# Kernel tuning notes

Hardware: AMD Instinct MI355X
Metric: run time of the kernel (lower is better)

The kernel has to match this reference:

```python
import jax, jax.numpy as jnp
import numpy as np

B, S, N = 8, 64, 256
STATE, IN_F, OUT_F = 128, 64, 64
ALPHA = 0.2
NEG = -9e15


def setup_inputs() -> dict:
    key = jax.random.key(0)
    ks = jax.random.split(key, 12)
    d = {
        "hyper_inputs": jax.random.normal(ks[0], (B, S, STATE), jnp.float32),
        "inputs": jax.random.normal(ks[1], (B, S, N, IN_F), jnp.float32),
        "Adj": jax.random.randint(ks[2], (N, N), 0, 2, jnp.int32),
        # hyper_w: Linear(STATE,32) -> ReLU -> Linear(32, OUT_F*IN_F)
        "w1": jax.random.normal(ks[3], (STATE, 32), jnp.float32) * 0.08,
        "b1": jax.random.normal(ks[4], (32,), jnp.float32) * 0.01,
        "w2": jax.random.normal(ks[5], (32, OUT_F * IN_F), jnp.float32) * 0.08,
        "b2": jax.random.normal(ks[6], (OUT_F * IN_F,), jnp.float32) * 0.01,
        # hyper_a: Linear(STATE,32) -> ReLU -> Linear(32, 2*OUT_F)
        "aw1": jax.random.normal(ks[7], (STATE, 32), jnp.float32) * 0.08,
        "ab1": jax.random.normal(ks[8], (32,), jnp.float32) * 0.01,
        "aw2": jax.random.normal(ks[9], (32, 2 * OUT_F), jnp.float32) * 0.08,
        "ab2": jax.random.normal(ks[10], (2 * OUT_F,), jnp.float32) * 0.01,
    }
    return d


def _leaky(x):
    return jnp.where(x >= 0, x, ALPHA * x)


def reference(hyper_inputs, inputs, Adj, w1, b1, w2, b2, aw1, ab1, aw2, ab2):
    # hypernetwork-generated per-(b,s) weights
    hdn = jax.nn.relu(hyper_inputs @ w1 + b1)            # [B,S,32]
    W = jnp.abs(hdn @ w2 + b2).reshape(B, S, IN_F, OUT_F)
    hda = jax.nn.relu(hyper_inputs @ aw1 + ab1)
    a = jnp.abs(hda @ aw2 + ab2)                          # [B,S,2*OUT_F]

    h = jnp.einsum('bsni,bsio->bsno', inputs, W)          # [B,S,N,OUT_F]

    # decomposed GAT scores: e[b,s,i,j] = leakyrelu(h_i.a1 + h_j.a2)
    a1, a2 = a[..., :OUT_F], a[..., OUT_F:]
    e1 = jnp.einsum('bsno,bso->bsn', h, a1)               # source term
    e2 = jnp.einsum('bsno,bso->bsn', h, a2)               # target term
    e = _leaky(e1[..., :, None] + e2[..., None, :])       # [B,S,N,N]

    attention = jnp.where(Adj > 0, e, NEG)
    # NOTE: faithful to original: softmax over dim=1 (the S axis)
    attention = jax.nn.softmax(attention, axis=1)
    h_prime = jnp.einsum('bsij,bsjo->bsio', attention, h)  # [B,S,N,OUT_F]
    return jax.nn.elu(h_prime)                              # concat=True branch
```

## Files before the change

kernel.cpp:

```cpp
#include <hip/hip_runtime.h>
#include <hip/hip_bf16.h>
#include <math.h>

#define BB 8
#define SS 64
#define NN 256
#define ST 128
#define IF 64
#define OF 64
#define H1 32
#define ALPHA 0.2f
#define LOG2E 1.4426950408889634f

typedef short short8 __attribute__((ext_vector_type(8)));
typedef short short4_t __attribute__((ext_vector_type(4)));
typedef float f32x4 __attribute__((ext_vector_type(4)));
typedef unsigned short ushort_t;

static __device__ __forceinline__ ushort_t f2bf(float f) {
    __hip_bfloat16 h = __float2bfloat16(f);
    return *reinterpret_cast<ushort_t*>(&h);
}

__global__ __launch_bounds__(512) void k_hyper2(
    const float* __restrict__ hyper,
    const float* __restrict__ w1, const float* __restrict__ b1,
    const float* __restrict__ w2, const float* __restrict__ b2,
    const float* __restrict__ aw1, const float* __restrict__ ab1,
    const float* __restrict__ aw2, const float* __restrict__ ab2,
    float* __restrict__ Wd, float* __restrict__ Aa)
{
    const int t = threadIdx.x;
    const int bs0 = blockIdx.x * 2;
    __shared__ float hy[2][ST];
    __shared__ float hdn_s[2][H1];
    __shared__ float hda_s[2][H1];
    if (t < 2 * ST)
        hy[t >> 7][t & 127] = hyper[(size_t)bs0 * ST + t];
    __syncthreads();
    if (t < 64) {
        const int q = t >> 5, c = t & 31;
        float acc = b1[c];
#pragma unroll 4
        for (int k = 0; k < ST; ++k) acc = fmaf(hy[q][k], w1[k * H1 + c], acc);
        hdn_s[q][c] = fmaxf(acc, 0.f);
    } else if (t < 128) {
        const int tt = t - 64;
        const int q = tt >> 5, c = tt & 31;
        float acc = ab1[c];
#pragma unroll 4
        for (int k = 0; k < ST; ++k) acc = fmaf(hy[q][k], aw1[k * H1 + c], acc);
        hda_s[q][c] = fmaxf(acc, 0.f);
    }
    __syncthreads();
    if (t < 256) {
        const int q = t >> 7, c = t & 127;
        float a = ab2[c];
#pragma unroll
        for (int k = 0; k < H1; ++k)
            a = fmaf(hda_s[q][k], aw2[k * 128 + c], a);
        Aa[(size_t)(bs0 + q) * 128 + c] = fabsf(a);
    }
#pragma unroll
    for (int p = 0; p < 2; ++p) {
        const int e = t * 4 + p * 2048;
        const float4 bb = *(const float4*)&b2[e];
        float4 a0 = bb, a1 = bb;
#pragma unroll
        for (int kq = 0; kq < 8; ++kq) {
            const float4 h0 = *(const float4*)&hdn_s[0][kq * 4];
            const float4 h1 = *(const float4*)&hdn_s[1][kq * 4];
#pragma unroll
            for (int c = 0; c < 4; ++c) {
                const float4 wv = *(const float4*)&w2[(size_t)(kq * 4 + c) * 4096 + e];
                const float s0 = (c == 0) ? h0.x : (c == 1) ? h0.y : (c == 2) ? h0.z : h0.w;
                const float s1 = (c == 0) ? h1.x : (c == 1) ? h1.y : (c == 2) ? h1.z : h1.w;
                a0.x = fmaf(s0, wv.x, a0.x); a0.y = fmaf(s0, wv.y, a0.y);
                a0.z = fmaf(s0, wv.z, a0.z); a0.w = fmaf(s0, wv.w, a0.w);
                a1.x = fmaf(s1, wv.x, a1.x); a1.y = fmaf(s1, wv.y, a1.y);
                a1.z = fmaf(s1, wv.z, a1.z); a1.w = fmaf(s1, wv.w, a1.w);
            }
        }
        a0.x = fabsf(a0.x); a0.y = fabsf(a0.y); a0.z = fabsf(a0.z); a0.w = fabsf(a0.w);
        a1.x = fabsf(a1.x); a1.y = fabsf(a1.y); a1.z = fabsf(a1.z); a1.w = fabsf(a1.w);
        *(float4*)&Wd[(size_t)(bs0 + 0) * 4096 + e] = a0;
        *(float4*)&Wd[(size_t)(bs0 + 1) * 4096 + e] = a1;
    }
}

__global__ __launch_bounds__(256) void k_h(
    const float* __restrict__ x, const float* __restrict__ Wd,
    const float* __restrict__ Aa,
    ushort_t* __restrict__ HbT, float* __restrict__ E1, float* __restrict__ E2)
{
    const int bs = blockIdx.x;
    const int tid = threadIdx.x;
    const int wid = tid >> 6;
    const int lane = tid & 63;
    const int l15 = lane & 15;
    const int lhi = lane >> 4;

    __shared__ ushort_t Wt[IF * OF];
    __shared__ float wa1s[IF], wa2s[IF];
    __shared__ float a1s[OF], a2s[OF];

    if (tid < 64) a1s[tid] = Aa[(size_t)bs * 128 + tid];
    else if (tid < 128) a2s[tid - 64] = Aa[(size_t)bs * 128 + tid];

    {
        const float4* w4 = (const float4*)(Wd + (size_t)bs * 4096);
#pragma unroll
        for (int p = 0; p < 4; ++p) {
            const int idx = tid + p * 256;
            const float4 f = w4[idx];
            const int k = (idx * 4) >> 6;
            const int o0 = (idx * 4) & 63;
            Wt[(o0 + 0) * 64 + (k ^ (((o0 + 0) & 7) << 3))] = f2bf(f.x);
            Wt[(o0 + 1) * 64 + (k ^ (((o0 + 1) & 7) << 3))] = f2bf(f.y);
            Wt[(o0 + 2) * 64 + (k ^ (((o0 + 2) & 7) << 3))] = f2bf(f.z);
            Wt[(o0 + 3) * 64 + (k ^ (((o0 + 3) & 7) << 3))] = f2bf(f.w);
        }
    }
    __syncthreads();

    if (tid < 64) {
        const float4* wr = (const float4*)(Wd + (size_t)bs * 4096 + tid * 64);
        float s1 = 0.f, s2 = 0.f;
#pragma unroll
        for (int q = 0; q < 16; ++q) {
            const float4 f = wr[q];
            const float4 u = *(const float4*)&a1s[q * 4];
            const float4 v = *(const float4*)&a2s[q * 4];
            s1 += f.x * u.x + f.y * u.y + f.z * u.z + f.w * u.w;
            s2 += f.x * v.x + f.y * v.y + f.z * v.z + f.w * v.w;
        }
        wa1s[tid] = s1; wa2s[tid] = s2;
    }
    __syncthreads();

    {
        const float4* xr = (const float4*)(x + ((size_t)bs * NN + tid) * IF);
        float s1 = 0.f, s2 = 0.f;
#pragma unroll
        for (int q = 0; q < 16; ++q) {
            const float4 f = xr[q];
            const float4 u = *(const float4*)&wa1s[q * 4];
            const float4 v = *(const float4*)&wa2s[q * 4];
            s1 += f.x * u.x + f.y * u.y + f.z * u.z + f.w * u.w;
            s2 += f.x * v.x + f.y * v.y + f.z * v.z + f.w * v.w;
        }
        E1[(size_t)bs * NN + tid] = s1 * LOG2E;
        E2[(size_t)bs * NN + tid] = s2 * LOG2E;
    }

    f32x4 acc[4][4];
#pragma unroll
    for (int mt = 0; mt < 4; ++mt)
#pragma unroll
        for (int nt = 0; nt < 4; ++nt) acc[mt][nt] = (f32x4){0.f, 0.f, 0.f, 0.f};

    short8 af[4][2];
#pragma unroll
    for (int mt = 0; mt < 4; ++mt) {
        const int row = wid * 64 + mt * 16 + l15;
        const float* xrow = x + ((size_t)bs * NN + row) * IF;
#pragma unroll
        for (int ks = 0; ks < 2; ++ks) {
            const int k0 = ks * 32 + lhi * 8;
            const float4 fa = *(const float4*)&xrow[k0];
            const float4 fb = *(const float4*)&xrow[k0 + 4];
            short8 pk;
            pk[0] = (short)f2bf(fa.x); pk[1] = (short)f2bf(fa.y);
            pk[2] = (short)f2bf(fa.z); pk[3] = (short)f2bf(fa.w);
            pk[4] = (short)f2bf(fb.x); pk[5] = (short)f2bf(fb.y);
            pk[6] = (short)f2bf(fb.z); pk[7] = (short)f2bf(fb.w);
            af[mt][ks] = pk;
        }
    }
    short8 bfr[4][2];
#pragma unroll
    for (int nt = 0; nt < 4; ++nt) {
        const int o = nt * 16 + l15;
#pragma unroll
        for (int ks = 0; ks < 2; ++ks) {
            const int k0 = ks * 32 + lhi * 8;
            bfr[nt][ks] = *(const short8*)&Wt[o * 64 + (k0 ^ ((o & 7) << 3))];
        }
    }
#pragma unroll
    for (int mt = 0; mt < 4; ++mt)
#pragma unroll
        for (int nt = 0; nt < 4; ++nt) {
            acc[mt][nt] = __builtin_amdgcn_mfma_f32_16x16x32_bf16(
                af[mt][0], bfr[nt][0], acc[mt][nt], 0, 0, 0);
            acc[mt][nt] = __builtin_amdgcn_mfma_f32_16x16x32_bf16(
                af[mt][1], bfr[nt][1], acc[mt][nt], 0, 0, 0);
        }

    ushort_t* hb = HbT + (size_t)bs * (OF * NN);
#pragma unroll
    for (int mt = 0; mt < 4; ++mt) {
        const int rbase = wid * 64 + mt * 16 + lhi * 4;
#pragma unroll
        for (int nt = 0; nt < 4; ++nt) {
            const int o = nt * 16 + l15;
            short4_t pk;
            pk[0] = (short)f2bf(acc[mt][nt][0]);
            pk[1] = (short)f2bf(acc[mt][nt][1]);
            pk[2] = (short)f2bf(acc[mt][nt][2]);
            pk[3] = (short)f2bf(acc[mt][nt][3]);
            *(short4_t*)(hb + (size_t)o * NN + rbase) = pk;
        }
    }
}

__global__ __launch_bounds__(256) void k_softstats(
    const float* __restrict__ E1, const float* __restrict__ E2,
    const int* __restrict__ Adj, unsigned int* __restrict__ MR)
{
    const int bid = blockIdx.x;
    const int b = bid >> 6, i0 = (bid & 63) * 4;
    const int t = threadIdx.x;
    __shared__ float e1s[4][SS];
    {
        const int ii = t >> 6, s = t & 63;
        e1s[ii][s] = E1[(size_t)(b * SS + s) * NN + i0 + ii];
    }
    float e2r[SS];
#pragma unroll
    for (int s = 0; s < SS; ++s)
        e2r[s] = E2[(size_t)(b * SS + s) * NN + t];
    __syncthreads();

#pragma unroll
    for (int ii = 0; ii < 4; ++ii) {
        float v[SS];
        float mx = -3.0e38f;
#pragma unroll
        for (int s = 0; s < SS; ++s) {
            float u = e1s[ii][s] + e2r[s];
            u = fmaxf(u, ALPHA * u);
            v[s] = u;
            mx = fmaxf(mx, u);
        }
        const unsigned int mu = (unsigned int)f2bf(mx);
        const float mUse = __uint_as_float(mu << 16);
        float sum = 0.f;
#pragma unroll
        for (int s = 0; s < SS; ++s)
            sum += exp2f(v[s] - mUse);
        const int adj = Adj[(size_t)(i0 + ii) * NN + t];
        const float r = (adj > 0) ? (1.f / sum) : -0.015625f;
        MR[(size_t)(b * NN + i0 + ii) * NN + t] =
            (mu << 16) | (unsigned int)f2bf(r);
    }
}

__global__ __launch_bounds__(512) void k_attn(
    const ushort_t* __restrict__ HbT, const float* __restrict__ E1,
    const float* __restrict__ E2, const unsigned int* __restrict__ MR,
    float* __restrict__ out)
{
    const int bs = blockIdx.x;
    const int b = bs >> 6;
    const int tid = threadIdx.x;
    const int wid = tid >> 6;
    const int lane = tid & 63;
    const int l15 = lane & 15;
    const int lhi = lane >> 4;

    __shared__ float e2s[NN];
    if (tid < NN) e2s[tid] = E2[(size_t)bs * NN + tid];
    __syncthreads();

    float e1r[2];
#pragma unroll
    for (int mt = 0; mt < 2; ++mt)
        e1r[mt] = E1[(size_t)bs * NN + wid * 32 + mt * 16 + l15];

    f32x4 acc[2][4];
#pragma unroll
    for (int mt = 0; mt < 2; ++mt)
#pragma unroll
        for (int nt = 0; nt < 4; ++nt) acc[mt][nt] = (f32x4){0.f, 0.f, 0.f, 0.f};

    const ushort_t* hb = HbT + (size_t)bs * (OF * NN);
    const unsigned int* mrb = MR + ((size_t)b * NN) * NN;
    const uint4* mrow0 = (const uint4*)(mrb + (size_t)(wid * 32 + l15) * NN);
    const uint4* mrow1 = (const uint4*)(mrb + (size_t)(wid * 32 + 16 + l15) * NN);

    for (int ch = 0; ch < 4; ++ch) {
        short8 bfr[4][2];
#pragma unroll
        for (int nt = 0; nt < 4; ++nt) {
            const int o = nt * 16 + l15;
#pragma unroll
            for (int ks = 0; ks < 2; ++ks) {
                const int j0 = ch * 64 + ks * 32 + lhi * 8;
                bfr[nt][ks] = *(const short8*)(hb + (size_t)o * NN + j0);
            }
        }
        uint4 mq[2][2][2];
#pragma unroll
        for (int ks = 0; ks < 2; ++ks) {
            const int qi = (ch * 64 + ks * 32 + lhi * 8) >> 2;
            mq[0][ks][0] = mrow0[qi]; mq[0][ks][1] = mrow0[qi + 1];
            mq[1][ks][0] = mrow1[qi]; mq[1][ks][1] = mrow1[qi + 1];
        }
        float e2v[2][8];
#pragma unroll
        for (int ks = 0; ks < 2; ++ks) {
            const int k0 = ch * 64 + ks * 32 + lhi * 8;
            const float4 lo = *(const float4*)&e2s[k0];
            const float4 hi = *(const float4*)&e2s[k0 + 4];
            e2v[ks][0] = lo.x; e2v[ks][1] = lo.y; e2v[ks][2] = lo.z; e2v[ks][3] = lo.w;
            e2v[ks][4] = hi.x; e2v[ks][5] = hi.y; e2v[ks][6] = hi.z; e2v[ks][7] = hi.w;
        }
#pragma unroll
        for (int mt = 0; mt < 2; ++mt) {
            const float e1v = e1r[mt];
            short8 af[2];
#pragma unroll
            for (int ks = 0; ks < 2; ++ks) {
                const unsigned int wv[8] = {
                    mq[mt][ks][0].x, mq[mt][ks][0].y, mq[mt][ks][0].z, mq[mt][ks][0].w,
                    mq[mt][ks][1].x, mq[mt][ks][1].y, mq[mt][ks][1].z, mq[mt][ks][1].w};
                short8 pk;
#pragma unroll
                for (int kk = 0; kk < 8; ++kk) {
                    const float Mf = __uint_as_float(wv[kk] & 0xFFFF0000u);
                    const float Rf = __uint_as_float(wv[kk] << 16);
                    float v = e1v + e2v[ks][kk];
                    v = fmaxf(v, ALPHA * v);
                    const float a = (Rf < 0.f) ? -Rf : exp2f(v - Mf) * Rf;
                    pk[kk] = (short)f2bf(a);
                }
                af[ks] = pk;
            }
#pragma unroll
            for (int nt = 0; nt < 4; ++nt) {
                acc[mt][nt] = __builtin_amdgcn_mfma_f32_16x16x32_bf16(
                    af[0], bfr[nt][0], acc[mt][nt], 0, 0, 0);
                acc[mt][nt] = __builtin_amdgcn_mfma_f32_16x16x32_bf16(
                    af[1], bfr[nt][1], acc[mt][nt], 0, 0, 0);
            }
        }
    }

    float* ob = out + (size_t)bs * (NN * OF);
#pragma unroll
    for (int mt = 0; mt < 2; ++mt) {
        const int rbase = wid * 32 + mt * 16 + lhi * 4;
#pragma unroll
        for (int nt = 0; nt < 4; ++nt) {
            const int o = nt * 16 + l15;
#pragma unroll
            for (int reg = 0; reg < 4; ++reg) {
                float v = acc[mt][nt][reg];
                v = (v > 0.f) ? v : (__expf(v) - 1.f);
                ob[(size_t)(rbase + reg) * OF + o] = v;
            }
        }
    }
}

extern "C" void kernel_launch(void* const* d_in, const int* in_sizes, int n_in,
                              void* d_out, int out_size, void* d_ws, size_t ws_size,
                              hipStream_t stream)
{
    const float* hyper = (const float*)d_in[0];
    const float* x     = (const float*)d_in[1];
    const int*   Adj   = (const int*)d_in[2];
    const float* w1    = (const float*)d_in[3];
    const float* b1    = (const float*)d_in[4];
    const float* w2    = (const float*)d_in[5];
    const float* b2    = (const float*)d_in[6];
    const float* aw1   = (const float*)d_in[7];
    const float* ab1   = (const float*)d_in[8];
    const float* aw2   = (const float*)d_in[9];
    const float* ab2   = (const float*)d_in[10];
    float* out = (float*)d_out;

    float* ws      = (float*)d_ws;
    float* Wd      = ws;
    float* Aa      = Wd + 2097152;
    ushort_t* HbT  = (ushort_t*)(Aa + 65536);
    float* E1      = (float*)(HbT + 8388608);
    float* E2      = E1 + 131072;
    unsigned int* MRp = (unsigned int*)(E2 + 131072);

    k_hyper2<<<dim3(256), dim3(512), 0, stream>>>(hyper, w1, b1, w2, b2,
                                                  aw1, ab1, aw2, ab2, Wd, Aa);
    k_h<<<dim3(512), dim3(256), 0, stream>>>(x, Wd, Aa, HbT, E1, E2);
    k_softstats<<<dim3(512), dim3(256), 0, stream>>>(E1, E2, Adj, MRp);
    k_attn<<<dim3(512), dim3(512), 0, stream>>>(HbT, E1, E2, MRp, out);
}
```

Measured before the change: 88.20 us.

## Store H and softmax stats in MFMA fragment-tiled layout for coalesced loads

The intermediate H (bf16, transposed) and the packed max/reciprocal buffer are now written in a tiled layout of 16 rows by 8 elements, matching the MFMA fragment each lane reads. The attention kernel's per-lane 16-byte loads become contiguous across lanes instead of striding by a full row. This targets uncoalesced global loads in the attention kernel. In exchange, the producer kernels now do more scattered writes: the stats writes in particular go from one row of 256 contiguous words to 8-word chunks per thread.

```diff
diff --git a/kernel.cpp b/kernel.cpp
--- a/kernel.cpp
+++ b/kernel.cpp
@@ -91,7 +91,7 @@
 __global__ __launch_bounds__(256) void k_h(
     const float* __restrict__ x, const float* __restrict__ Wd,
     const float* __restrict__ Aa,
-    ushort_t* __restrict__ HbT, float* __restrict__ E1, float* __restrict__ E2)
+    ushort_t* __restrict__ HbTw, float* __restrict__ E1, float* __restrict__ E2)
 {
     const int bs = blockIdx.x;
     const int tid = threadIdx.x;
@@ -197,26 +197,26 @@
                 af[mt][1], bfr[nt][1], acc[mt][nt], 0, 0, 0);
         }
 
-    ushort_t* hb = HbT + (size_t)bs * (OF * NN);
+    ushort_t* hbw = HbTw + (size_t)bs * (OF * NN);
 #pragma unroll
     for (int mt = 0; mt < 4; ++mt) {
-        const int rbase = wid * 64 + mt * 16 + lhi * 4;
+        const int nb = wid * 8 + mt * 2 + (lhi >> 1);
+        const int ne = (lhi & 1) * 4;
 #pragma unroll
         for (int nt = 0; nt < 4; ++nt) {
-            const int o = nt * 16 + l15;
             short4_t pk;
             pk[0] = (short)f2bf(acc[mt][nt][0]);
             pk[1] = (short)f2bf(acc[mt][nt][1]);
             pk[2] = (short)f2bf(acc[mt][nt][2]);
             pk[3] = (short)f2bf(acc[mt][nt][3]);
-            *(short4_t*)(hb + (size_t)o * NN + rbase) = pk;
+            *(short4_t*)(hbw + ((size_t)(nt * 32 + nb) * 16 + l15) * 8 + ne) = pk;
         }
     }
 }
 
 __global__ __launch_bounds__(256) void k_softstats(
     const float* __restrict__ E1, const float* __restrict__ E2,
-    const int* __restrict__ Adj, unsigned int* __restrict__ MR)
+    const int* __restrict__ Adj, unsigned int* __restrict__ MRw)
 {
     const int bid = blockIdx.x;
     const int b = bid >> 6, i0 = (bid & 63) * 4;
@@ -249,16 +249,17 @@
 #pragma unroll
         for (int s = 0; s < SS; ++s)
             sum += exp2f(v[s] - mUse);
-        const int adj = Adj[(size_t)(i0 + ii) * NN + t];
+        const int i = i0 + ii;
+        const int adj = Adj[(size_t)i * NN + t];
         const float r = (adj > 0) ? (1.f / sum) : -0.015625f;
-        MR[(size_t)(b * NN + i0 + ii) * NN + t] =
-            (mu << 16) | (unsigned int)f2bf(r);
+        MRw[((((size_t)b * 16 + (i >> 4)) * 32 + (t >> 3)) * 16 + (i & 15)) * 8
+            + (t & 7)] = (mu << 16) | (unsigned int)f2bf(r);
     }
 }
 
 __global__ __launch_bounds__(512) void k_attn(
-    const ushort_t* __restrict__ HbT, const float* __restrict__ E1,
-    const float* __restrict__ E2, const unsigned int* __restrict__ MR,
+    const ushort_t* __restrict__ HbTw, const float* __restrict__ E1,
+    const float* __restrict__ E2, const unsigned int* __restrict__ MRw,
     float* __restrict__ out)
 {
     const int bs = blockIdx.x;
@@ -284,28 +285,30 @@
 #pragma unroll
         for (int nt = 0; nt < 4; ++nt) acc[mt][nt] = (f32x4){0.f, 0.f, 0.f, 0.f};
 
-    const ushort_t* hb = HbT + (size_t)bs * (OF * NN);
-    const unsigned int* mrb = MR + ((size_t)b * NN) * NN;
-    const uint4* mrow0 = (const uint4*)(mrb + (size_t)(wid * 32 + l15) * NN);
-    const uint4* mrow1 = (const uint4*)(mrb + (size_t)(wid * 32 + 16 + l15) * NN);
+    const ushort_t* hbw = HbTw + (size_t)bs * (OF * NN);
+    const unsigned int* mrb = MRw + (size_t)b * (NN * NN);
+    const unsigned int* mr0 = mrb + ((size_t)(wid * 2 + 0) * 32) * 128 + l15 * 8;
+    const unsigned int* mr1 = mrb + ((size_t)(wid * 2 + 1) * 32) * 128 + l15 * 8;
 
     for (int ch = 0; ch < 4; ++ch) {
         short8 bfr[4][2];
 #pragma unroll
         for (int nt = 0; nt < 4; ++nt) {
-            const int o = nt * 16 + l15;
 #pragma unroll
             for (int ks = 0; ks < 2; ++ks) {
-                const int j0 = ch * 64 + ks * 32 + lhi * 8;
-                bfr[nt][ks] = *(const short8*)(hb + (size_t)o * NN + j0);
+                const int nb = ch * 8 + ks * 4 + lhi;
+                bfr[nt][ks] = *(const short8*)(hbw
+                    + ((size_t)(nt * 32 + nb) * 16 + l15) * 8);
             }
         }
         uint4 mq[2][2][2];
 #pragma unroll
         for (int ks = 0; ks < 2; ++ks) {
-            const int qi = (ch * 64 + ks * 32 + lhi * 8) >> 2;
-            mq[0][ks][0] = mrow0[qi]; mq[0][ks][1] = mrow0[qi + 1];
-            mq[1][ks][0] = mrow1[qi]; mq[1][ks][1] = mrow1[qi + 1];
+            const int kb = ch * 8 + ks * 4 + lhi;
+            mq[0][ks][0] = *(const uint4*)(mr0 + kb * 128);
+            mq[0][ks][1] = *(const uint4*)(mr0 + kb * 128 + 4);
+            mq[1][ks][0] = *(const uint4*)(mr1 + kb * 128);
+            mq[1][ks][1] = *(const uint4*)(mr1 + kb * 128 + 4);
         }
         float e2v[2][8];
 #pragma unroll
@@ -384,14 +387,14 @@
     float* ws      = (float*)d_ws;
     float* Wd      = ws;
     float* Aa      = Wd + 2097152;
-    ushort_t* HbT  = (ushort_t*)(Aa + 65536);
-    float* E1      = (float*)(HbT + 8388608);
+    ushort_t* HbTw = (ushort_t*)(Aa + 65536);
+    float* E1      = (float*)(HbTw + 8388608);
     float* E2      = E1 + 131072;
-    unsigned int* MRp = (unsigned int*)(E2 + 131072);
+    unsigned int* MRw = (unsigned int*)(E2 + 131072);
 
     k_hyper2<<<dim3(256), dim3(512), 0, stream>>>(hyper, w1, b1, w2, b2,
                                                   aw1, ab1, aw2, ab2, Wd, Aa);
-    k_h<<<dim3(512), dim3(256), 0, stream>>>(x, Wd, Aa, HbT, E1, E2);
-    k_softstats<<<dim3(512), dim3(256), 0, stream>>>(E1, E2, Adj, MRp);
-    k_attn<<<dim3(512), dim3(512), 0, stream>>>(HbT, E1, E2, MRp, out);
-}
+    k_h<<<dim3(512), dim3(256), 0, stream>>>(x, Wd, Aa, HbTw, E1, E2);
+    k_softstats<<<dim3(512), dim3(256), 0, stream>>>(E1, E2, Adj, MRw);
+    k_attn<<<dim3(512), dim3(512), 0, stream>>>(HbTw, E1, E2, MRw, out);
+}
```

After: 75.23 us. -14.7%, faster.
